# Kernel tuning notes

Hardware: AMD Instinct MI355X
Metric: run time of the kernel (lower is better)

The kernel has to match this reference:

```python
import jax, jax.numpy as jnp
import numpy as np

B, IN1, IN2, D, H, E, K = 16384, 1024, 1024, 1024, 2048, 8, 2
EPS = 1e-5  # torch BatchNorm1d / LayerNorm default eps


def setup_inputs() -> dict:
    key = jax.random.key(0)
    ks = jax.random.split(key, 24)
    s = 0.02

    def W(k, o, i):
        return jax.random.normal(k, (o, i), jnp.float32) * s

    def b(k, o):
        return jax.random.normal(k, (o,), jnp.float32) * s

    return {
        "x1": jax.random.normal(ks[0], (B, IN1), jnp.float32),
        "x2": jax.random.normal(ks[1], (B, IN2), jnp.float32),
        # projections
        "p1_w": W(ks[2], D, IN1), "p1_b": b(ks[3], D),
        "p2_w": W(ks[4], D, IN2), "p2_b": b(ks[5], D),
        # MLP interaction (eval-mode BN: running_mean=0, running_var=1)
        "m1_w": W(ks[6], H, 2 * D), "m1_b": b(ks[7], H),
        "bn1_g": 1.0 + 0.1 * jax.random.normal(ks[8], (H,), jnp.float32),
        "bn1_b": 0.1 * jax.random.normal(ks[9], (H,), jnp.float32),
        "m2_w": W(ks[10], H, H), "m2_b": b(ks[11], H),
        "bn2_g": 1.0 + 0.1 * jax.random.normal(ks[12], (H,), jnp.float32),
        "bn2_b": 0.1 * jax.random.normal(ks[13], (H,), jnp.float32),
        "m3_w": W(ks[14], 2 * D, H), "m3_b": b(ks[15], 2 * D),
        "ln_g": 1.0 + 0.1 * jax.random.normal(ks[16], (2 * D,), jnp.float32),
        "ln_b": 0.1 * jax.random.normal(ks[17], (2 * D,), jnp.float32),
        # shared MoE (used for both x1 and x2 branches)
        "ex_w": jax.random.normal(ks[18], (E, D, D), jnp.float32) * s,  # [E, out, in]
        "ex_b": jax.random.normal(ks[19], (E, D), jnp.float32) * s,
        "gate_w": W(ks[20], E, D), "gate_b": b(ks[20], E),
        # fusion head
        "fus_w": W(ks[21], D, 2 * D), "fus_b": b(ks[21], D),
        "bnf_g": 1.0 + 0.1 * jax.random.normal(ks[22], (D,), jnp.float32),
        "bnf_b": 0.1 * jax.random.normal(ks[22], (D,), jnp.float32),
        "reg_w": W(ks[23], 1, D), "reg_b": b(ks[23], 1),
    }


def _bn_eval(x, g, b):
    # BatchNorm1d in eval mode with running_mean=0, running_var=1
    return x * (g / np.sqrt(1.0 + EPS)) + b


def _ln(x, g, b):
    mu = jnp.mean(x, axis=-1, keepdims=True)
    var = jnp.mean(jnp.square(x - mu), axis=-1, keepdims=True)
    return (x - mu) * jax.lax.rsqrt(var + EPS) * g + b


def reference(x1, x2, p1_w, p1_b, p2_w, p2_b,
              m1_w, m1_b, bn1_g, bn1_b, m2_w, m2_b, bn2_g, bn2_b,
              m3_w, m3_b, ln_g, ln_b,
              ex_w, ex_b, gate_w, gate_b,
              fus_w, fus_b, bnf_g, bnf_b, reg_w, reg_b):
    # dual projections (seq_len is structurally 1; keep tensors 2-D [B, D])
    x1p = x1 @ p1_w.T + p1_b
    x2p = x2 @ p2_w.T + p2_b

    # MLP interaction layer
    h = jnp.concatenate([x1p, x2p], axis=1)              # [B, 2D]
    h = jax.nn.relu(_bn_eval(h @ m1_w.T + m1_b, bn1_g, bn1_b))
    h = jax.nn.relu(_bn_eval(h @ m2_w.T + m2_b, bn2_g, bn2_b))
    mlp_out = _ln(h @ m3_w.T + m3_b, ln_g, ln_b)         # [B, 2D]
    x1m, x2m = mlp_out[:, :D], mlp_out[:, D:]

    def moe(x):  # x: [B, D]
        logits = x @ gate_w.T + gate_b                   # [B, E]
        vals, idx = jax.lax.top_k(logits, K)             # [B, K]
        gw = jax.nn.softmax(vals, axis=1)                # softmax over top-k only
        eo = jnp.einsum('ni,eoi->neo', x, ex_w) + ex_b   # [B, E, D] all experts
        sel = jnp.take_along_axis(eo, idx[:, :, None], axis=1)  # [B, K, D]
        return jnp.sum(sel * gw[:, :, None], axis=1)     # [B, D]

    fused = jnp.concatenate([moe(x1m), moe(x2m)], axis=1) @ fus_w.T + fus_b
    fused = _bn_eval(fused, bnf_g, bnf_b)                # dropout is identity in eval
    return fused @ reg_w.T + reg_b                       # [B, 1]
```

## Files before the change

kernel.cpp:

```cpp
#include <hip/hip_runtime.h>
#include <stdint.h>
#include <math.h>

#define BROWS 16384

typedef _Float16 h8 __attribute__((ext_vector_type(8)));
typedef _Float16 h4 __attribute__((ext_vector_type(4)));
typedef __bf16   b8 __attribute__((ext_vector_type(8)));
typedef __bf16   b4 __attribute__((ext_vector_type(4)));
typedef float    f4 __attribute__((ext_vector_type(4)));

typedef __attribute__((address_space(3))) char       lds_char;
typedef __attribute__((address_space(1))) const char gbl_char;

__device__ __forceinline__ void gload16(const void* g, void* l) {
  __builtin_amdgcn_global_load_lds((const gbl_char*)(uintptr_t)g,
                                   (lds_char*)(uintptr_t)l, 16, 0, 0);
}


template<int EPI>
__global__ __launch_bounds__(256, 2)
void gemm_split(const _Float16* __restrict__ Ah, const _Float16* __restrict__ Al,
                const _Float16* __restrict__ Wh, const _Float16* __restrict__ Wl,
                const _Float16* __restrict__ WhB, const _Float16* __restrict__ WlB,
                const int lda, const int ldw, const int K,
                _Float16* __restrict__ Ch, _Float16* __restrict__ Cl,
                float* __restrict__ Cf, const int ldc,
                const float* __restrict__ v0, const float* __restrict__ v1,
                const float* __restrict__ v0B, const int zoff)
{
  __shared__ char smem[65536];
  char* const sAh = smem;
  char* const sAl = smem + 16384;
  char* const sWh = smem + 32768;
  char* const sWl = smem + 49152;

  if (blockIdx.z) {
    Wh = WhB; Wl = WlB; v0 = v0B;
    Ah += zoff; Al += zoff; Ch += zoff; Cl += zoff;
  }

  const int tid  = threadIdx.x;
  const int wid  = tid >> 6, lane = tid & 63;
  const int bm = blockIdx.x, bn = blockIdx.y;
  const int wr = wid >> 1, wc = wid & 1;
  const int sr  = lane >> 3;
  const int scb = ((lane & 7) ^ sr) * 16;
  const int fr  = lane & 15;
  const int sw0 = ((lane >> 4) ^ (lane & 7)) * 16;
  const int sw1 = ((4 + (lane >> 4)) ^ (lane & 7)) * 16;

  f4 accA[4][4] = {};
  f4 accB[4][4] = {};

  const size_t arow0 = (size_t)bm * 128;
  const size_t wrow0 = (size_t)bn * 128;

  for (int k0 = 0; k0 < K; k0 += 64) {
    __syncthreads();
#pragma unroll
    for (int i = 0; i < 4; ++i) {
      const int rb = wid * 32 + i * 8;
      const size_t ga = (arow0 + rb + sr) * (size_t)lda + k0;
      const size_t gw = (wrow0 + rb + sr) * (size_t)ldw + k0;
      const int lo = rb * 128;
      gload16((const char*)(Ah + ga) + scb, sAh + lo);
      gload16((const char*)(Al + ga) + scb, sAl + lo);
      gload16((const char*)(Wh + gw) + scb, sWh + lo);
      gload16((const char*)(Wl + gw) + scb, sWl + lo);
    }
    __syncthreads();

#pragma unroll
    for (int ks = 0; ks < 2; ++ks) {
      const int sw = ks ? sw1 : sw0;
      h8 ah[4], al[4], bh[4], bl[4];
#pragma unroll
      for (int mi = 0; mi < 4; ++mi) {
        const int r = (wr * 64 + mi * 16 + fr) * 128 + sw;
        ah[mi] = *(const h8*)(sAh + r);
        al[mi] = *(const h8*)(sAl + r);
      }
#pragma unroll
      for (int ni = 0; ni < 4; ++ni) {
        const int r = (wc * 64 + ni * 16 + fr) * 128 + sw;
        bh[ni] = *(const h8*)(sWh + r);
        bl[ni] = *(const h8*)(sWl + r);
      }
#pragma unroll
      for (int mi = 0; mi < 4; ++mi)
#pragma unroll
        for (int ni = 0; ni < 4; ++ni) {
          accA[mi][ni] = __builtin_amdgcn_mfma_f32_16x16x32_f16(ah[mi], bh[ni], accA[mi][ni], 0, 0, 0);
          accB[mi][ni] = __builtin_amdgcn_mfma_f32_16x16x32_f16(ah[mi], bl[ni], accB[mi][ni], 0, 0, 0);
          accB[mi][ni] = __builtin_amdgcn_mfma_f32_16x16x32_f16(al[mi], bh[ni], accB[mi][ni], 0, 0, 0);
        }
    }
  }

  const int rg = (lane >> 4) * 4;
#pragma unroll
  for (int mi = 0; mi < 4; ++mi)
#pragma unroll
    for (int ni = 0; ni < 4; ++ni) {
      const int gcol = bn * 128 + wc * 64 + ni * 16 + fr;
      const float a0 = v0[gcol];
      const float a1 = (EPI == 1) ? v1[gcol] : 0.f;
#pragma unroll
      for (int j = 0; j < 4; ++j) {
        const size_t grow = arow0 + wr * 64 + mi * 16 + rg + j;
        float y = accA[mi][ni][j] + accB[mi][ni][j] * (1.f / 2048.f);
        const size_t off = grow * (size_t)ldc + gcol;
        if constexpr (EPI == 0) {
          y += a0;
          const _Float16 hh = (_Float16)y;
          Ch[off] = hh;
          Cl[off] = (_Float16)((y - (float)hh) * 2048.f);
        } else if constexpr (EPI == 1) {
          y = fmaxf(fmaf(y, a0, a1), 0.f);
          const _Float16 hh = (_Float16)y;
          Ch[off] = hh;
          Cl[off] = (_Float16)((y - (float)hh) * 2048.f);
        } else {
          Cf[off] = y + a0;
        }
      }
    }
}

__global__ __launch_bounds__(256, 2)
void gemm_fus(const __bf16* __restrict__ A, const __bf16* __restrict__ W,
              const int lda, const int ldw, const int K,
              float* __restrict__ Cf, const int ldc,
              const float* __restrict__ v0, const float* __restrict__ v1)
{
  __shared__ char smem[32768];
  char* const sA = smem;
  char* const sW = smem + 16384;

  const int tid  = threadIdx.x;
  const int wid  = tid >> 6, lane = tid & 63;
  const int bm = blockIdx.x, bn = blockIdx.y;
  const int wr = wid >> 1, wc = wid & 1;
  const int sr  = lane >> 3;
  const int scb = ((lane & 7) ^ sr) * 16;
  const int fr  = lane & 15;
  const int sw0 = ((lane >> 4) ^ (lane & 7)) * 16;
  const int sw1 = ((4 + (lane >> 4)) ^ (lane & 7)) * 16;

  f4 acc[4][4] = {};

  const size_t arow0 = (size_t)bm * 128;
  const size_t wrow0 = (size_t)bn * 128;

  for (int k0 = 0; k0 < K; k0 += 64) {
    __syncthreads();
#pragma unroll
    for (int i = 0; i < 4; ++i) {
      const int rb = wid * 32 + i * 8;
      const size_t ga = (arow0 + rb + sr) * (size_t)lda + k0;
      const size_t gw = (wrow0 + rb + sr) * (size_t)ldw + k0;
      const int lo = rb * 128;
      gload16((const char*)(A + ga) + scb, sA + lo);
      gload16((const char*)(W + gw) + scb, sW + lo);
    }
    __syncthreads();

#pragma unroll
    for (int ks = 0; ks < 2; ++ks) {
      const int sw = ks ? sw1 : sw0;
      b8 av[4], bv[4];
#pragma unroll
      for (int mi = 0; mi < 4; ++mi)
        av[mi] = *(const b8*)(sA + (wr * 64 + mi * 16 + fr) * 128 + sw);
#pragma unroll
      for (int ni = 0; ni < 4; ++ni)
        bv[ni] = *(const b8*)(sW + (wc * 64 + ni * 16 + fr) * 128 + sw);
#pragma unroll
      for (int mi = 0; mi < 4; ++mi)
#pragma unroll
        for (int ni = 0; ni < 4; ++ni)
          acc[mi][ni] = __builtin_amdgcn_mfma_f32_16x16x32_bf16(av[mi], bv[ni], acc[mi][ni], 0, 0, 0);
    }
  }

  const int rg = (lane >> 4) * 4;
#pragma unroll
  for (int mi = 0; mi < 4; ++mi)
#pragma unroll
    for (int j = 0; j < 4; ++j) {
      const size_t grow = arow0 + wr * 64 + mi * 16 + rg + j;
#pragma unroll
      for (int ni = 0; ni < 4; ++ni) {
        const int gcol = bn * 128 + wc * 64 + ni * 16 + fr;
        Cf[grow * (size_t)ldc + gcol] = fmaf(acc[mi][ni][j], v0[gcol], v1[gcol]);
      }
    }
}

template<int PASS>
__global__ __launch_bounds__(256, 2)
void gemm_moe(const __bf16* __restrict__ A,
              const __bf16* __restrict__ Wall,
              const int* __restrict__ lrow, const float* __restrict__ lw,
              const int* __restrict__ blkexp,
              const float* __restrict__ eb,
              float* __restrict__ ACC,
              __bf16* __restrict__ BFBh)
{
  const int bx = blockIdx.x, by = blockIdx.y;
  const int e = blkexp[bx];
  if (e < 0) return;

  __shared__ char smem[32768];
  __shared__ int   slrow[128];
  __shared__ float slw[128];
  char* const sA = smem;
  char* const sW = smem + 16384;

  const int tid  = threadIdx.x;
  const int wid  = tid >> 6, lane = tid & 63;
  if (tid < 128) { slrow[tid] = lrow[bx * 128 + tid]; slw[tid] = lw[bx * 128 + tid]; }
  __syncthreads();

  const __bf16* W = Wall + (size_t)e * 1048576 + (size_t)by * 131072;

  const int wr = wid >> 1, wc = wid & 1;
  const int sr  = lane >> 3;
  const int scb = ((lane & 7) ^ sr) * 16;
  const int fr  = lane & 15;
  const int sw0 = ((lane >> 4) ^ (lane & 7)) * 16;
  const int sw1 = ((4 + (lane >> 4)) ^ (lane & 7)) * 16;

  const char* abase[4];
#pragma unroll
  for (int i = 0; i < 4; ++i) {
    int s = slrow[wid * 32 + i * 8 + sr];
    if (s < 0) s = 0;
    abase[i] = (const char*)(A + (size_t)s * 2048) + scb;
  }

  f4 acc[4][4] = {};

  for (int k0 = 0; k0 < 1024; k0 += 64) {
    __syncthreads();
#pragma unroll
    for (int i = 0; i < 4; ++i) {
      const int rb = wid * 32 + i * 8;
      const int lo = rb * 128;
      gload16(abase[i] + (size_t)k0 * 2, sA + lo);
      gload16((const char*)(W + (size_t)(rb + sr) * 1024 + k0) + scb, sW + lo);
    }
    __syncthreads();

#pragma unroll
    for (int ks = 0; ks < 2; ++ks) {
      const int sw = ks ? sw1 : sw0;
      b8 av[4], bv[4];
#pragma unroll
      for (int mi = 0; mi < 4; ++mi)
        av[mi] = *(const b8*)(sA + (wr * 64 + mi * 16 + fr) * 128 + sw);
#pragma unroll
      for (int ni = 0; ni < 4; ++ni)
        bv[ni] = *(const b8*)(sW + (wc * 64 + ni * 16 + fr) * 128 + sw);
#pragma unroll
      for (int mi = 0; mi < 4; ++mi)
#pragma unroll
        for (int ni = 0; ni < 4; ++ni)
          acc[mi][ni] = __builtin_amdgcn_mfma_f32_16x16x32_bf16(av[mi], bv[ni], acc[mi][ni], 0, 0, 0);
    }
  }

  const int rg = (lane >> 4) * 4;
  const float* ebp = eb + (size_t)e * 1024;
#pragma unroll
  for (int mi = 0; mi < 4; ++mi)
#pragma unroll
    for (int j = 0; j < 4; ++j) {
      const int local = wr * 64 + mi * 16 + rg + j;
      const int R = slrow[local];
      if (R < 0) continue;
      const float w = slw[local];
#pragma unroll
      for (int ni = 0; ni < 4; ++ni) {
        const int gcol = by * 128 + wc * 64 + ni * 16 + fr;
        const float v = w * (acc[mi][ni][j] + ebp[gcol]);
        if constexpr (PASS == 0) {
          ACC[(size_t)R * 1024 + gcol] = v;
        } else {
          BFBh[(size_t)R * 2048 + gcol] = (__bf16)(ACC[(size_t)R * 1024 + gcol] + v);
        }
      }
    }
}


__global__ void split_w(const float* __restrict__ src, _Float16* __restrict__ dh,
                        _Float16* __restrict__ dl, const size_t n)
{
  const size_t i = ((size_t)blockIdx.x * 256 + threadIdx.x) * 4;
  if (i >= n) return;
  const f4 v = *(const f4*)(src + i);
  h4 hh, ll;
#pragma unroll
  for (int j = 0; j < 4; ++j) {
    const _Float16 h = (_Float16)v[j];
    hh[j] = h;
    ll[j] = (_Float16)((v[j] - (float)h) * 2048.f);
  }
  *(h4*)(dh + i) = hh;
  *(h4*)(dl + i) = ll;
}

__global__ void cvt_bf(const float* __restrict__ src, __bf16* __restrict__ dst, const size_t n)
{
  const size_t i = ((size_t)blockIdx.x * 256 + threadIdx.x) * 4;
  if (i >= n) return;
  const f4 v = *(const f4*)(src + i);
  b4 o;
#pragma unroll
  for (int j = 0; j < 4; ++j) o[j] = (__bf16)v[j];
  *(b4*)(dst + i) = o;
}

__global__ void prep_x(const float* __restrict__ x1, const float* __restrict__ x2,
                       _Float16* __restrict__ ph, _Float16* __restrict__ pl)
{
  const size_t i = ((size_t)blockIdx.x * 256 + threadIdx.x) * 4;
  const int b = (int)(i >> 11);
  const int c = (int)(i & 2047);
  const float* s = (c < 1024) ? (x1 + (size_t)b * 1024 + c)
                              : (x2 + (size_t)b * 1024 + (c - 1024));
  const f4 v = *(const f4*)s;
  h4 hh, ll;
#pragma unroll
  for (int j = 0; j < 4; ++j) {
    const _Float16 h = (_Float16)v[j];
    hh[j] = h;
    ll[j] = (_Float16)((v[j] - (float)h) * 2048.f);
  }
  *(h4*)(ph + i) = hh;
  *(h4*)(pl + i) = ll;
}

__global__ void fold_kernel(const float* g1, const float* b1, const float* mb1,
                            const float* g2, const float* b2, const float* mb2,
                            const float* gf, const float* bf, const float* fb,
                            float* s1, float* t1, float* s2, float* t2,
                            float* fs, float* ft)
{
  const int t = blockIdx.x * 256 + threadIdx.x;
  const float inv = (float)(1.0 / sqrt(1.0 + 1.0e-5));
  if (t < 2048) {
    float a = g1[t] * inv; s1[t] = a; t1[t] = mb1[t] * a + b1[t];
    float c = g2[t] * inv; s2[t] = c; t2[t] = mb2[t] * c + b2[t];
  }
  if (t < 1024) {
    float a = gf[t] * inv; fs[t] = a; ft[t] = fb[t] * a + bf[t];
  }
}

__global__ __launch_bounds__(256)
void ln_gate_kernel(const float* __restrict__ xf, __bf16* __restrict__ xb,
                    const float* __restrict__ lg, const float* __restrict__ lb,
                    const float* __restrict__ gw, const float* __restrict__ gb,
                    int* __restrict__ sel, float* __restrict__ selw,
                    const int rowbase, const int CM2)
{
  const int row = blockIdx.x;
  const float* xr = xf + (size_t)row * 2048;
  const int tid = threadIdx.x;
  const int wid = tid >> 6, lane = tid & 63;
  const f4 v0 = *(const f4*)(xr + tid * 4);
  const f4 v1 = *(const f4*)(xr + 1024 + tid * 4);
  double s = 0.0, ss = 0.0;
#pragma unroll
  for (int j = 0; j < 4; ++j) {
    s  += (double)v0[j] + (double)v1[j];
    ss += (double)v0[j] * v0[j] + (double)v1[j] * v1[j];
  }
#pragma unroll
  for (int o = 32; o; o >>= 1) { s += __shfl_xor(s, o); ss += __shfl_xor(ss, o); }
  __shared__ double red[8];
  if (!lane) { red[wid] = s; red[4 + wid] = ss; }
  __syncthreads();
  const double S  = red[0] + red[1] + red[2] + red[3];
  const double SS = red[4] + red[5] + red[6] + red[7];
  const double mu = S * (1.0 / 2048.0);
  const double var = SS * (1.0 / 2048.0) - mu * mu;
  const float inv = (float)(1.0 / sqrt(var + 1.0e-5));
  const float muf = (float)mu;
  f4 o0, o1;
  b4 q0, q1;
#pragma unroll
  for (int j = 0; j < 4; ++j) {
    const int c0 = tid * 4 + j, c1 = 1024 + tid * 4 + j;
    o0[j] = (v0[j] - muf) * inv * lg[c0] + lb[c0];
    o1[j] = (v1[j] - muf) * inv * lg[c1] + lb[c1];
    q0[j] = (__bf16)o0[j];
    q1[j] = (__bf16)o1[j];
  }
  *(b4*)(xb + (size_t)row * 2048 + tid * 4) = q0;
  *(b4*)(xb + (size_t)row * 2048 + 1024 + tid * 4) = q1;

  double l0[8], l1[8];
#pragma unroll
  for (int e = 0; e < 8; ++e) {
    const f4 w = *(const f4*)(gw + e * 1024 + tid * 4);
    l0[e] = (double)(o0[0] * w[0]) + (double)(o0[1] * w[1])
          + (double)(o0[2] * w[2]) + (double)(o0[3] * w[3]);
    l1[e] = (double)(o1[0] * w[0]) + (double)(o1[1] * w[1])
          + (double)(o1[2] * w[2]) + (double)(o1[3] * w[3]);
  }
#pragma unroll
  for (int o = 32; o; o >>= 1)
#pragma unroll
    for (int e = 0; e < 8; ++e) {
      l0[e] += __shfl_xor(l0[e], o);
      l1[e] += __shfl_xor(l1[e], o);
    }
  __shared__ double red2[4][16];
  if (!lane)
#pragma unroll
    for (int e = 0; e < 8; ++e) { red2[wid][e] = l0[e]; red2[wid][8 + e] = l1[e]; }
  __syncthreads();
  if (tid < 2) {
    const int h = tid;
    double lg8[8];
#pragma unroll
    for (int e = 0; e < 8; ++e)
      lg8[e] = red2[0][h * 8 + e] + red2[1][h * 8 + e] + red2[2][h * 8 + e]
             + red2[3][h * 8 + e] + (double)gb[e];
    int i0 = 0;
    for (int e = 1; e < 8; ++e) if (lg8[e] > lg8[i0]) i0 = e;
    int i1 = -1;
    for (int e = 0; e < 8; ++e) if (e != i0 && (i1 < 0 || lg8[e] > lg8[i1])) i1 = e;
    const double p = exp(lg8[i1] - lg8[i0]);
    const double z = 1.0 + p;
    int* sp = sel + h * CM2 + (size_t)(rowbase + row) * 2;
    float* wp = selw + h * CM2 + (size_t)(rowbase + row) * 2;
    sp[0] = i0; wp[0] = (float)(1.0 / z);
    sp[1] = i1; wp[1] = (float)(p / z);
  }
}

__global__ void count_kernel(const int* __restrict__ sel, int* __restrict__ cnt,
                             const int CM)
{
  const int idx = blockIdx.x * 256 + threadIdx.x;
  const bool valid = idx < 2 * CM;
  const int h = (idx / CM) & 1;
  const int lane = threadIdx.x & 63;
#pragma unroll
  for (int r = 0; r < 2; ++r) {
    const int e = valid ? sel[idx * 2 + r] : -1;
    const int g = h * 2 + r;
    for (int ee = 0; ee < 8; ++ee) {
      const unsigned long long mask = __ballot(e == ee);
      if (mask && lane == __ffsll((unsigned long long)mask) - 1)
        atomicAdd(&cnt[g * 8 + ee], __popcll(mask));
    }
  }
}

__global__ void prefix_kernel(const int* __restrict__ cnt, int* __restrict__ cursor,
                              int* __restrict__ blkexp, const int NBLK)
{
  const int tid = threadIdx.x;
  for (int i = tid; i < 4 * NBLK; i += 256) blkexp[i] = -1;
  __syncthreads();
  if (tid < 32) {
    const int g = tid >> 3, e = tid & 7;
    int off = 0;
    for (int j = 0; j < e; ++j) off += ((cnt[g * 8 + j] + 127) >> 7) << 7;
    cursor[g * 8 + e] = off;
    const int nb = (cnt[g * 8 + e] + 127) >> 7;
    for (int b = 0; b < nb; ++b) blkexp[g * NBLK + (off >> 7) + b] = e;
  }
}

__global__ void scatter_kernel(const int* __restrict__ sel, const float* __restrict__ selw,
                               int* __restrict__ cursor,
                               int* __restrict__ lrow, float* __restrict__ lw,
                               const int CM, const int LCAP)
{
  const int idx = blockIdx.x * 256 + threadIdx.x;
  const bool valid = idx < 2 * CM;
  const int h = (idx / CM) & 1;
  const int R = valid ? (idx - (idx / CM) * CM) : 0;
  const int lane = threadIdx.x & 63;
#pragma unroll
  for (int r = 0; r < 2; ++r) {
    const int e = valid ? sel[idx * 2 + r] : -1;
    const int g = h * 2 + r;
    int pos = -1;
    for (int ee = 0; ee < 8; ++ee) {
      const unsigned long long mask = __ballot(e == ee);
      if (mask) {
        const int leader = __ffsll((unsigned long long)mask) - 1;
        int base = 0;
        if (lane == leader) base = atomicAdd(&cursor[g * 8 + ee], __popcll(mask));
        base = __shfl(base, leader);
        if (e == ee)
          pos = base + __popcll(mask & ((1ull << lane) - 1ull));
      }
    }
    if (valid) {
      lrow[g * LCAP + pos] = R;
      lw[g * LCAP + pos] = selw[idx * 2 + r];
    }
  }
}

__global__ __launch_bounds__(256)
void reg_kernel(const float* __restrict__ xf, const float* __restrict__ rw,
                const float* __restrict__ rb, float* __restrict__ out)
{
  const int wid = threadIdx.x >> 6, lane = threadIdx.x & 63;
  const int row = blockIdx.x * 4 + wid;
  const float* xr = xf + (size_t)row * 1024;
  double acc = 0.0;
#pragma unroll
  for (int i = 0; i < 4; ++i) {
    const int f = (lane + 64 * i) * 4;
    const f4 a = *(const f4*)(xr + f);
    const f4 w = *(const f4*)(rw + f);
    acc += (double)a[0] * w[0] + (double)a[1] * w[1] + (double)a[2] * w[2] + (double)a[3] * w[3];
  }
#pragma unroll
  for (int o = 32; o; o >>= 1) acc += __shfl_xor(acc, o);
  if (!lane) out[row] = (float)(acc + (double)rb[0]);
}


extern "C" void kernel_launch(void* const* d_in, const int* in_sizes, int n_in,
                              void* d_out, int out_size, void* d_ws, size_t ws_size,
                              hipStream_t stream)
{
  (void)in_sizes; (void)n_in; (void)out_size;
  const float* x1    = (const float*)d_in[0];
  const float* x2    = (const float*)d_in[1];
  const float* p1_w  = (const float*)d_in[2];
  const float* p1_b  = (const float*)d_in[3];
  const float* p2_w  = (const float*)d_in[4];
  const float* p2_b  = (const float*)d_in[5];
  const float* m1_w  = (const float*)d_in[6];
  const float* m1_b  = (const float*)d_in[7];
  const float* bn1_g = (const float*)d_in[8];
  const float* bn1_b = (const float*)d_in[9];
  const float* m2_w  = (const float*)d_in[10];
  const float* m2_b  = (const float*)d_in[11];
  const float* bn2_g = (const float*)d_in[12];
  const float* bn2_b = (const float*)d_in[13];
  const float* m3_w  = (const float*)d_in[14];
  const float* m3_b  = (const float*)d_in[15];
  const float* ln_g  = (const float*)d_in[16];
  const float* ln_b  = (const float*)d_in[17];
  const float* ex_w  = (const float*)d_in[18];
  const float* ex_b  = (const float*)d_in[19];
  const float* gate_w= (const float*)d_in[20];
  const float* gate_b= (const float*)d_in[21];
  const float* fus_w = (const float*)d_in[22];
  const float* fus_b = (const float*)d_in[23];
  const float* bnf_g = (const float*)d_in[24];
  const float* bnf_b = (const float*)d_in[25];
  const float* reg_w = (const float*)d_in[26];
  const float* reg_b = (const float*)d_in[27];

  char* ws = (char*)d_ws;
  size_t off = 0;
  auto alloc = [&](size_t bytes) { size_t o = off; off += (bytes + 255) & ~(size_t)255; return o; };

  const size_t oWHp1 = alloc((size_t)1048576 * 2), oWLp1 = alloc((size_t)1048576 * 2);
  const size_t oWHp2 = alloc((size_t)1048576 * 2), oWLp2 = alloc((size_t)1048576 * 2);
  const size_t oWHm1 = alloc((size_t)4194304 * 2), oWLm1 = alloc((size_t)4194304 * 2);
  const size_t oWHm2 = alloc((size_t)4194304 * 2), oWLm2 = alloc((size_t)4194304 * 2);
  const size_t oWHm3 = alloc((size_t)4194304 * 2), oWLm3 = alloc((size_t)4194304 * 2);
  const size_t oS1 = alloc(2048 * 4), oT1 = alloc(2048 * 4);
  const size_t oS2 = alloc(2048 * 4), oT2 = alloc(2048 * 4);
  const size_t oFS = alloc(1024 * 4), oFT = alloc(1024 * 4);
  const size_t oCnt = alloc(32 * 4), oCur = alloc(32 * 4);
  const size_t fixedEnd = off;

  int CM = BROWS;
  while (CM > 2048) {
    const int ct = (CM < 4096) ? CM : 4096;
    const size_t nblk = (size_t)CM / 128 + 8;
    const size_t lcap = nblk * 128;
    const size_t need = fixedEnd
                      + 4 * ((size_t)ct * 4096 + 256)
                      + 2 * ((size_t)CM * 4096 + 256)
                      + 2 * ((size_t)CM * 16 + 256)
                      + 2 * (4 * lcap * 4 + 256)
                      + (4 * nblk * 4 + 256) + 8192;
    if (ws_size >= need) break;
    CM >>= 1;
  }
  const int CT = (CM < 4096) ? CM : 4096;
  const int NBLK = CM / 128 + 8;
  const int LCAP = NBLK * 128;

  const size_t oP    = alloc(4 * (size_t)CT * 4096);
  const size_t oBFA  = alloc((size_t)CM * 4096);
  const size_t oBFB  = alloc((size_t)CM * 4096);
  const size_t oSel  = alloc((size_t)CM * 16);
  const size_t oSelw = alloc((size_t)CM * 16);
  const size_t oLrow = alloc((size_t)4 * LCAP * 4);
  const size_t oLw   = alloc((size_t)4 * LCAP * 4);
  const size_t oBlk  = alloc((size_t)4 * NBLK * 4);

  _Float16* WHp1 = (_Float16*)(ws + oWHp1); _Float16* WLp1 = (_Float16*)(ws + oWLp1);
  _Float16* WHp2 = (_Float16*)(ws + oWHp2); _Float16* WLp2 = (_Float16*)(ws + oWLp2);
  _Float16* WHm1 = (_Float16*)(ws + oWHm1); _Float16* WLm1 = (_Float16*)(ws + oWLm1);
  _Float16* WHm2 = (_Float16*)(ws + oWHm2); _Float16* WLm2 = (_Float16*)(ws + oWLm2);
  _Float16* WHm3 = (_Float16*)(ws + oWHm3); _Float16* WLm3 = (_Float16*)(ws + oWLm3);
  __bf16* WBex = (__bf16*)(ws + oWHm1);
  __bf16* WBfu = (__bf16*)(ws + oWHm2);
  _Float16* PH0 = (_Float16*)(ws + oP);
  _Float16* PL0 = (_Float16*)(ws + oP + (size_t)CT * 4096);
  _Float16* PH1 = (_Float16*)(ws + oP + 2 * (size_t)CT * 4096);
  _Float16* PL1 = (_Float16*)(ws + oP + 3 * (size_t)CT * 4096);
  float* F32    = (float*)(ws + oP);
  float* ACC    = (float*)(ws + oP);
  float* F32fus = (float*)(ws + oP);
  __bf16* BFA = (__bf16*)(ws + oBFA);
  __bf16* BFB = (__bf16*)(ws + oBFB);
  int*   sel  = (int*)(ws + oSel);
  float* selw = (float*)(ws + oSelw);
  int*   lrow = (int*)(ws + oLrow);
  float* lw   = (float*)(ws + oLw);
  int*   blkexp = (int*)(ws + oBlk);
  int*   cnt = (int*)(ws + oCnt);
  int*   cur = (int*)(ws + oCur);
  float* s1v = (float*)(ws + oS1); float* t1v = (float*)(ws + oT1);
  float* s2v = (float*)(ws + oS2); float* t2v = (float*)(ws + oT2);
  float* fsv = (float*)(ws + oFS); float* ftv = (float*)(ws + oFT);

  const dim3 T(256);
  fold_kernel<<<8, T, 0, stream>>>(bn1_g, bn1_b, m1_b, bn2_g, bn2_b, m2_b,
                                   bnf_g, bnf_b, fus_b, s1v, t1v, s2v, t2v, fsv, ftv);
  split_w<<<1024, T, 0, stream>>>(p1_w, WHp1, WLp1, 1048576);
  split_w<<<1024, T, 0, stream>>>(p2_w, WHp2, WLp2, 1048576);

  const dim3 GP(CT / 128, 8, 2), GT16(CT / 128, 16, 1), GM(NBLK, 8), GF(CM / 128, 8);
  for (int m0 = 0; m0 < BROWS; m0 += CM) {
    split_w<<<4096, T, 0, stream>>>(m1_w, WHm1, WLm1, 4194304);
    split_w<<<4096, T, 0, stream>>>(m2_w, WHm2, WLm2, 4194304);
    split_w<<<4096, T, 0, stream>>>(m3_w, WHm3, WLm3, 4194304);

    for (int r0 = 0; r0 < CM; r0 += CT) {
      const float* x1c = x1 + (size_t)(m0 + r0) * 1024;
      const float* x2c = x2 + (size_t)(m0 + r0) * 1024;
      prep_x<<<CT * 2, T, 0, stream>>>(x1c, x2c, PH0, PL0);
      gemm_split<0><<<GP, T, 0, stream>>>(PH0, PL0, WHp1, WLp1, WHp2, WLp2,
                                          2048, 1024, 1024,
                                          PH1, PL1, nullptr, 2048,
                                          p1_b, nullptr, p2_b, 1024);
      gemm_split<1><<<GT16, T, 0, stream>>>(PH1, PL1, WHm1, WLm1, WHm1, WLm1,
                                            2048, 2048, 2048,
                                            PH0, PL0, nullptr, 2048,
                                            s1v, t1v, s1v, 0);
      gemm_split<1><<<GT16, T, 0, stream>>>(PH0, PL0, WHm2, WLm2, WHm2, WLm2,
                                            2048, 2048, 2048,
                                            PH1, PL1, nullptr, 2048,
                                            s2v, t2v, s2v, 0);
      gemm_split<2><<<GT16, T, 0, stream>>>(PH1, PL1, WHm3, WLm3, WHm3, WLm3,
                                            2048, 2048, 2048,
                                            nullptr, nullptr, F32, 2048,
                                            m3_b, nullptr, m3_b, 0);
      ln_gate_kernel<<<CT, T, 0, stream>>>(F32, BFA + (size_t)r0 * 2048,
                                           ln_g, ln_b, gate_w, gate_b,
                                           sel, selw, r0, CM * 2);
    }

    cvt_bf<<<8192, T, 0, stream>>>(ex_w, WBex, 8388608);
    cvt_bf<<<2048, T, 0, stream>>>(fus_w, WBfu, 2097152);

    hipMemsetAsync(cnt, 0, 32 * 4, stream);
    count_kernel<<<(2 * CM + 255) / 256, T, 0, stream>>>(sel, cnt, CM);
    prefix_kernel<<<1, T, 0, stream>>>(cnt, cur, blkexp, NBLK);
    hipMemsetAsync(lrow, 0xFF, (size_t)4 * LCAP * 4, stream);
    scatter_kernel<<<(2 * CM + 255) / 256, T, 0, stream>>>(sel, selw, cur, lrow, lw, CM, LCAP);
    for (int h = 0; h < 2; ++h) {
      const int g0 = h * 2, g1 = h * 2 + 1;
      gemm_moe<0><<<GM, T, 0, stream>>>(BFA + h * 1024, WBex,
                                        lrow + (size_t)g0 * LCAP, lw + (size_t)g0 * LCAP,
                                        blkexp + g0 * NBLK, ex_b, ACC, nullptr);
      gemm_moe<1><<<GM, T, 0, stream>>>(BFA + h * 1024, WBex,
                                        lrow + (size_t)g1 * LCAP, lw + (size_t)g1 * LCAP,
                                        blkexp + g1 * NBLK, ex_b, ACC, BFB + h * 1024);
    }

    gemm_fus<<<GF, T, 0, stream>>>(BFB, WBfu, 2048, 2048, 2048, F32fus, 1024, fsv, ftv);
    reg_kernel<<<CM / 4, T, 0, stream>>>(F32fus, reg_w, reg_b, (float*)d_out + m0);
  }
}
```

Before: 1.882 ms.

## Switch GEMMs to 32x32x16 MFMA and compute gate logits in float

All three GEMM kernels (split-fp16, fusion, MoE) move from 16x16x32 MFMA tiles to 32x32x16 tiles. Each wave now issues fewer, larger MFMAs with fewer LDS fragment loads per k-step, and the LDS swizzle and epilogue row mapping are updated to match. The LN+gate kernel also computes the gating logits and their reductions in float instead of double, which removes slow FP64 arithmetic. The float gate logits could change top-k expert selection when two logits are nearly tied.

```diff
diff --git a/kernel.cpp b/kernel.cpp
--- a/kernel.cpp
+++ b/kernel.cpp
@@ -9,6 +9,7 @@
 typedef __bf16   b8 __attribute__((ext_vector_type(8)));
 typedef __bf16   b4 __attribute__((ext_vector_type(4)));
 typedef float    f4 __attribute__((ext_vector_type(4)));
+typedef float    f16v __attribute__((ext_vector_type(16)));
 
 typedef __attribute__((address_space(3))) char       lds_char;
 typedef __attribute__((address_space(1))) const char gbl_char;
@@ -47,12 +48,12 @@
   const int wr = wid >> 1, wc = wid & 1;
   const int sr  = lane >> 3;
   const int scb = ((lane & 7) ^ sr) * 16;
-  const int fr  = lane & 15;
-  const int sw0 = ((lane >> 4) ^ (lane & 7)) * 16;
-  const int sw1 = ((4 + (lane >> 4)) ^ (lane & 7)) * 16;
-
-  f4 accA[4][4] = {};
-  f4 accB[4][4] = {};
+  const int fb  = lane & 31;
+  const int fx  = lane >> 5;
+  const int s7  = lane & 7;
+
+  f16v accA[2][2] = {};
+  f16v accB[2][2] = {};
 
   const size_t arow0 = (size_t)bm * 128;
   const size_t wrow0 = (size_t)bn * 128;
@@ -73,44 +74,44 @@
     __syncthreads();
 
 #pragma unroll
-    for (int ks = 0; ks < 2; ++ks) {
-      const int sw = ks ? sw1 : sw0;
-      h8 ah[4], al[4], bh[4], bl[4];
-#pragma unroll
-      for (int mi = 0; mi < 4; ++mi) {
-        const int r = (wr * 64 + mi * 16 + fr) * 128 + sw;
+    for (int ks = 0; ks < 4; ++ks) {
+      const int sw = ((ks * 2 + fx) ^ s7) * 16;
+      h8 ah[2], al[2], bh[2], bl[2];
+#pragma unroll
+      for (int mi = 0; mi < 2; ++mi) {
+        const int r = (wr * 64 + mi * 32 + fb) * 128 + sw;
         ah[mi] = *(const h8*)(sAh + r);
         al[mi] = *(const h8*)(sAl + r);
       }
 #pragma unroll
-      for (int ni = 0; ni < 4; ++ni) {
-        const int r = (wc * 64 + ni * 16 + fr) * 128 + sw;
+      for (int ni = 0; ni < 2; ++ni) {
+        const int r = (wc * 64 + ni * 32 + fb) * 128 + sw;
         bh[ni] = *(const h8*)(sWh + r);
         bl[ni] = *(const h8*)(sWl + r);
       }
 #pragma unroll
-      for (int mi = 0; mi < 4; ++mi)
-#pragma unroll
-        for (int ni = 0; ni < 4; ++ni) {
-          accA[mi][ni] = __builtin_amdgcn_mfma_f32_16x16x32_f16(ah[mi], bh[ni], accA[mi][ni], 0, 0, 0);
-          accB[mi][ni] = __builtin_amdgcn_mfma_f32_16x16x32_f16(ah[mi], bl[ni], accB[mi][ni], 0, 0, 0);
-          accB[mi][ni] = __builtin_amdgcn_mfma_f32_16x16x32_f16(al[mi], bh[ni], accB[mi][ni], 0, 0, 0);
+      for (int mi = 0; mi < 2; ++mi)
+#pragma unroll
+        for (int ni = 0; ni < 2; ++ni) {
+          accA[mi][ni] = __builtin_amdgcn_mfma_f32_32x32x16_f16(ah[mi], bh[ni], accA[mi][ni], 0, 0, 0);
+          accB[mi][ni] = __builtin_amdgcn_mfma_f32_32x32x16_f16(ah[mi], bl[ni], accB[mi][ni], 0, 0, 0);
+          accB[mi][ni] = __builtin_amdgcn_mfma_f32_32x32x16_f16(al[mi], bh[ni], accB[mi][ni], 0, 0, 0);
         }
     }
   }
 
-  const int rg = (lane >> 4) * 4;
-#pragma unroll
-  for (int mi = 0; mi < 4; ++mi)
-#pragma unroll
-    for (int ni = 0; ni < 4; ++ni) {
-      const int gcol = bn * 128 + wc * 64 + ni * 16 + fr;
+#pragma unroll
+  for (int mi = 0; mi < 2; ++mi)
+#pragma unroll
+    for (int ni = 0; ni < 2; ++ni) {
+      const int gcol = bn * 128 + wc * 64 + ni * 32 + fb;
       const float a0 = v0[gcol];
       const float a1 = (EPI == 1) ? v1[gcol] : 0.f;
 #pragma unroll
-      for (int j = 0; j < 4; ++j) {
-        const size_t grow = arow0 + wr * 64 + mi * 16 + rg + j;
-        float y = accA[mi][ni][j] + accB[mi][ni][j] * (1.f / 2048.f);
+      for (int r = 0; r < 16; ++r) {
+        const int row32 = (r & 3) + 8 * (r >> 2) + 4 * fx;
+        const size_t grow = arow0 + wr * 64 + mi * 32 + row32;
+        float y = accA[mi][ni][r] + accB[mi][ni][r] * (1.f / 2048.f);
         const size_t off = grow * (size_t)ldc + gcol;
         if constexpr (EPI == 0) {
           y += a0;
@@ -145,11 +146,11 @@
   const int wr = wid >> 1, wc = wid & 1;
   const int sr  = lane >> 3;
   const int scb = ((lane & 7) ^ sr) * 16;
-  const int fr  = lane & 15;
-  const int sw0 = ((lane >> 4) ^ (lane & 7)) * 16;
-  const int sw1 = ((4 + (lane >> 4)) ^ (lane & 7)) * 16;
-
-  f4 acc[4][4] = {};
+  const int fb  = lane & 31;
+  const int fx  = lane >> 5;
+  const int s7  = lane & 7;
+
+  f16v acc[2][2] = {};
 
   const size_t arow0 = (size_t)bm * 128;
   const size_t wrow0 = (size_t)bn * 128;
@@ -168,33 +169,33 @@
     __syncthreads();
 
 #pragma unroll
-    for (int ks = 0; ks < 2; ++ks) {
-      const int sw = ks ? sw1 : sw0;
-      b8 av[4], bv[4];
-#pragma unroll
-      for (int mi = 0; mi < 4; ++mi)
-        av[mi] = *(const b8*)(sA + (wr * 64 + mi * 16 + fr) * 128 + sw);
-#pragma unroll
-      for (int ni = 0; ni < 4; ++ni)
-        bv[ni] = *(const b8*)(sW + (wc * 64 + ni * 16 + fr) * 128 + sw);
-#pragma unroll
-      for (int mi = 0; mi < 4; ++mi)
-#pragma unroll
-        for (int ni = 0; ni < 4; ++ni)
-          acc[mi][ni] = __builtin_amdgcn_mfma_f32_16x16x32_bf16(av[mi], bv[ni], acc[mi][ni], 0, 0, 0);
-    }
-  }
-
-  const int rg = (lane >> 4) * 4;
-#pragma unroll
-  for (int mi = 0; mi < 4; ++mi)
-#pragma unroll
-    for (int j = 0; j < 4; ++j) {
-      const size_t grow = arow0 + wr * 64 + mi * 16 + rg + j;
-#pragma unroll
-      for (int ni = 0; ni < 4; ++ni) {
-        const int gcol = bn * 128 + wc * 64 + ni * 16 + fr;
-        Cf[grow * (size_t)ldc + gcol] = fmaf(acc[mi][ni][j], v0[gcol], v1[gcol]);
+    for (int ks = 0; ks < 4; ++ks) {
+      const int sw = ((ks * 2 + fx) ^ s7) * 16;
+      b8 av[2], bv[2];
+#pragma unroll
+      for (int mi = 0; mi < 2; ++mi)
+        av[mi] = *(const b8*)(sA + (wr * 64 + mi * 32 + fb) * 128 + sw);
+#pragma unroll
+      for (int ni = 0; ni < 2; ++ni)
+        bv[ni] = *(const b8*)(sW + (wc * 64 + ni * 32 + fb) * 128 + sw);
+#pragma unroll
+      for (int mi = 0; mi < 2; ++mi)
+#pragma unroll
+        for (int ni = 0; ni < 2; ++ni)
+          acc[mi][ni] = __builtin_amdgcn_mfma_f32_32x32x16_bf16(av[mi], bv[ni], acc[mi][ni], 0, 0, 0);
+    }
+  }
+
+#pragma unroll
+  for (int mi = 0; mi < 2; ++mi)
+#pragma unroll
+    for (int ni = 0; ni < 2; ++ni) {
+      const int gcol = bn * 128 + wc * 64 + ni * 32 + fb;
+#pragma unroll
+      for (int r = 0; r < 16; ++r) {
+        const int row32 = (r & 3) + 8 * (r >> 2) + 4 * fx;
+        const size_t grow = arow0 + wr * 64 + mi * 32 + row32;
+        Cf[grow * (size_t)ldc + gcol] = fmaf(acc[mi][ni][r], v0[gcol], v1[gcol]);
       }
     }
 }
@@ -229,9 +230,9 @@
   const int wr = wid >> 1, wc = wid & 1;
   const int sr  = lane >> 3;
   const int scb = ((lane & 7) ^ sr) * 16;
-  const int fr  = lane & 15;
-  const int sw0 = ((lane >> 4) ^ (lane & 7)) * 16;
-  const int sw1 = ((4 + (lane >> 4)) ^ (lane & 7)) * 16;
+  const int fb  = lane & 31;
+  const int fx  = lane >> 5;
+  const int s7  = lane & 7;
 
   const char* abase[4];
 #pragma unroll
@@ -241,7 +242,7 @@
     abase[i] = (const char*)(A + (size_t)s * 2048) + scb;
   }
 
-  f4 acc[4][4] = {};
+  f16v acc[2][2] = {};
 
   for (int k0 = 0; k0 < 1024; k0 += 64) {
     __syncthreads();
@@ -255,37 +256,37 @@
     __syncthreads();
 
 #pragma unroll
-    for (int ks = 0; ks < 2; ++ks) {
-      const int sw = ks ? sw1 : sw0;
-      b8 av[4], bv[4];
-#pragma unroll
-      for (int mi = 0; mi < 4; ++mi)
-        av[mi] = *(const b8*)(sA + (wr * 64 + mi * 16 + fr) * 128 + sw);
-#pragma unroll
-      for (int ni = 0; ni < 4; ++ni)
-        bv[ni] = *(const b8*)(sW + (wc * 64 + ni * 16 + fr) * 128 + sw);
-#pragma unroll
-      for (int mi = 0; mi < 4; ++mi)
-#pragma unroll
-        for (int ni = 0; ni < 4; ++ni)
-          acc[mi][ni] = __builtin_amdgcn_mfma_f32_16x16x32_bf16(av[mi], bv[ni], acc[mi][ni], 0, 0, 0);
-    }
-  }
-
-  const int rg = (lane >> 4) * 4;
+    for (int ks = 0; ks < 4; ++ks) {
+      const int sw = ((ks * 2 + fx) ^ s7) * 16;
+      b8 av[2], bv[2];
+#pragma unroll
+      for (int mi = 0; mi < 2; ++mi)
+        av[mi] = *(const b8*)(sA + (wr * 64 + mi * 32 + fb) * 128 + sw);
+#pragma unroll
+      for (int ni = 0; ni < 2; ++ni)
+        bv[ni] = *(const b8*)(sW + (wc * 64 + ni * 32 + fb) * 128 + sw);
+#pragma unroll
+      for (int mi = 0; mi < 2; ++mi)
+#pragma unroll
+        for (int ni = 0; ni < 2; ++ni)
+          acc[mi][ni] = __builtin_amdgcn_mfma_f32_32x32x16_bf16(av[mi], bv[ni], acc[mi][ni], 0, 0, 0);
+    }
+  }
+
   const float* ebp = eb + (size_t)e * 1024;
 #pragma unroll
-  for (int mi = 0; mi < 4; ++mi)
-#pragma unroll
-    for (int j = 0; j < 4; ++j) {
-      const int local = wr * 64 + mi * 16 + rg + j;
+  for (int mi = 0; mi < 2; ++mi)
+#pragma unroll
+    for (int r = 0; r < 16; ++r) {
+      const int row32 = (r & 3) + 8 * (r >> 2) + 4 * fx;
+      const int local = wr * 64 + mi * 32 + row32;
       const int R = slrow[local];
       if (R < 0) continue;
       const float w = slw[local];
 #pragma unroll
-      for (int ni = 0; ni < 4; ++ni) {
-        const int gcol = by * 128 + wc * 64 + ni * 16 + fr;
-        const float v = w * (acc[mi][ni][j] + ebp[gcol]);
+      for (int ni = 0; ni < 2; ++ni) {
+        const int gcol = by * 128 + wc * 64 + ni * 32 + fb;
+        const float v = w * (acc[mi][ni][r] + ebp[gcol]);
         if constexpr (PASS == 0) {
           ACC[(size_t)R * 1024 + gcol] = v;
         } else {
@@ -404,14 +405,12 @@
   *(b4*)(xb + (size_t)row * 2048 + tid * 4) = q0;
   *(b4*)(xb + (size_t)row * 2048 + 1024 + tid * 4) = q1;
 
-  double l0[8], l1[8];
+  float l0[8], l1[8];
 #pragma unroll
   for (int e = 0; e < 8; ++e) {
     const f4 w = *(const f4*)(gw + e * 1024 + tid * 4);
-    l0[e] = (double)(o0[0] * w[0]) + (double)(o0[1] * w[1])
-          + (double)(o0[2] * w[2]) + (double)(o0[3] * w[3]);
-    l1[e] = (double)(o1[0] * w[0]) + (double)(o1[1] * w[1])
-          + (double)(o1[2] * w[2]) + (double)(o1[3] * w[3]);
+    l0[e] = o0[0] * w[0] + o0[1] * w[1] + o0[2] * w[2] + o0[3] * w[3];
+    l1[e] = o1[0] * w[0] + o1[1] * w[1] + o1[2] * w[2] + o1[3] * w[3];
   }
 #pragma unroll
   for (int o = 32; o; o >>= 1)
@@ -420,23 +419,23 @@
       l0[e] += __shfl_xor(l0[e], o);
       l1[e] += __shfl_xor(l1[e], o);
     }
-  __shared__ double red2[4][16];
+  __shared__ float red2[4][16];
   if (!lane)
 #pragma unroll
     for (int e = 0; e < 8; ++e) { red2[wid][e] = l0[e]; red2[wid][8 + e] = l1[e]; }
   __syncthreads();
   if (tid < 2) {
     const int h = tid;
-    double lg8[8];
+    float lg8[8];
 #pragma unroll
     for (int e = 0; e < 8; ++e)
       lg8[e] = red2[0][h * 8 + e] + red2[1][h * 8 + e] + red2[2][h * 8 + e]
-             + red2[3][h * 8 + e] + (double)gb[e];
+             + red2[3][h * 8 + e] + gb[e];
     int i0 = 0;
     for (int e = 1; e < 8; ++e) if (lg8[e] > lg8[i0]) i0 = e;
     int i1 = -1;
     for (int e = 0; e < 8; ++e) if (e != i0 && (i1 < 0 || lg8[e] > lg8[i1])) i1 = e;
-    const double p = exp(lg8[i1] - lg8[i0]);
+    const double p = exp((double)lg8[i1] - (double)lg8[i0]);
     const double z = 1.0 + p;
     int* sp = sel + h * CM2 + (size_t)(rowbase + row) * 2;
     float* wp = selw + h * CM2 + (size_t)(rowbase + row) * 2;
```

Measured after the change: 2.060 ms. +9.5%, slower.
